# Kernel tuning notes

Hardware: AMD Instinct MI355X
Metric: run time of the kernel (lower is better)

## Reference

```python
import jax, jax.numpy as jnp
import numpy as np

N_NODES = 65536
N_EDGES = 1048576
BN_EPS = 1e-5


def _glorot(key, shape):
    fan_in, fan_out = shape[0], shape[1]
    lim = np.sqrt(6.0 / (fan_in + fan_out))
    return jax.random.uniform(key, shape, jnp.float32, -lim, lim)


def setup_inputs() -> dict:
    key = jax.random.key(0)
    ks = jax.random.split(key, 16)
    inp = {}
    inp['x'] = jax.random.normal(ks[0], (N_NODES, 3), jnp.float32)
    inp['edge_src'] = jax.random.randint(ks[1], (N_EDGES,), 0, N_NODES, jnp.int32)
    inp['edge_dst'] = jax.random.randint(ks[2], (N_EDGES,), 0, N_NODES, jnp.int32)
    inp['edge_val'] = jax.random.uniform(ks[3], (N_EDGES,), jnp.float32)
    inp['num_pts'] = 1024  # points per shape (equal-size split)
    # GraphConvolution params: out = adj @ (x @ W) + b
    inp['gc1_w'] = _glorot(ks[4], (3, 64));     inp['gc1_b'] = jnp.zeros((64,), jnp.float32)
    inp['gc2_w'] = _glorot(ks[5], (64, 64));    inp['gc2_b'] = jnp.zeros((64,), jnp.float32)
    inp['gc3_w'] = _glorot(ks[6], (64, 1024));  inp['gc3_b'] = jnp.zeros((1024,), jnp.float32)
    # MLP head: Linear(1024,512)+BN+ReLU, Linear(512,256)+BN+ReLU, Linear(256,40)
    inp['fc1_w'] = _glorot(ks[7], (1024, 512)); inp['fc1_b'] = jnp.zeros((512,), jnp.float32)
    inp['bn1_g'] = jnp.ones((512,), jnp.float32); inp['bn1_b'] = jnp.zeros((512,), jnp.float32)
    inp['fc2_w'] = _glorot(ks[8], (512, 256));  inp['fc2_b'] = jnp.zeros((256,), jnp.float32)
    inp['bn2_g'] = jnp.ones((256,), jnp.float32); inp['bn2_b'] = jnp.zeros((256,), jnp.float32)
    inp['fc3_w'] = _glorot(ks[9], (256, 40));   inp['fc3_b'] = jnp.zeros((40,), jnp.float32)
    return inp


def _gcn_layer(x, w, b, src, dst, val):
    # adj @ (x @ W) + b, adj given as COO edge list (dst <- src weighted by val)
    support = x @ w                                   # [N, F_out]
    msg = support[src] * val[:, None]                 # gather + scale
    agg = jax.ops.segment_sum(msg, dst, num_segments=N_NODES)
    return agg + b


def _batchnorm(x, gamma, beta):
    mean = jnp.mean(x, axis=0)
    var = jnp.mean(jnp.square(x - mean), axis=0)  # biased var (torch train mode)
    return (x - mean) * jax.lax.rsqrt(var + BN_EPS) * gamma + beta


def reference(x, edge_src, edge_dst, edge_val, num_pts,
              gc1_w, gc1_b, gc2_w, gc2_b, gc3_w, gc3_b,
              fc1_w, fc1_b, bn1_g, bn1_b, fc2_w, fc2_b, bn2_g, bn2_b, fc3_w, fc3_b):
    h = jax.nn.relu(_gcn_layer(x, gc1_w, gc1_b, edge_src, edge_dst, edge_val))
    h = jax.nn.relu(_gcn_layer(h, gc2_w, gc2_b, edge_src, edge_dst, edge_val))
    h = jax.nn.relu(_gcn_layer(h, gc3_w, gc3_b, edge_src, edge_dst, edge_val))
    # per-shape max pool: split into equal-size shapes along node dim
    n_shapes = N_NODES // num_pts
    global_feat = jnp.max(h.reshape(n_shapes, num_pts, 1024), axis=1)  # [B, 1024]
    # MLP head with train-mode BatchNorm
    z = jax.nn.relu(_batchnorm(global_feat @ fc1_w + fc1_b, bn1_g, bn1_b))
    z = jax.nn.relu(_batchnorm(z @ fc2_w + fc2_b, bn2_g, bn2_b))
    scores = z @ fc3_w + fc3_b                         # [B, 40]
    return jax.nn.log_softmax(scores, axis=-1)
```

## Files before the change

### kernel.cpp

```cpp
#include <hip/hip_runtime.h>
#include <math.h>

#define NN 65536
#define NE 1048576
#define CAP 17408
#define PCAP 24576

typedef __attribute__((ext_vector_type(8))) short short8;
typedef __attribute__((ext_vector_type(4))) float f32x4;

__device__ inline unsigned short f2bf(float f) {
  unsigned u = __float_as_uint(f);
  unsigned r = u + 0x7fff + ((u >> 16) & 1);
  return (unsigned short)(r >> 16);
}
__device__ inline float bf2f(unsigned short h) { return __uint_as_float(((unsigned)h) << 16); }

__global__ __launch_bounds__(256) void k_prep(const float* __restrict__ x, float4* __restrict__ x4,
                                              int* __restrict__ gcur, const float* __restrict__ w3,
                                              unsigned short* __restrict__ bfrag, unsigned* __restrict__ gf) {
  int bid = blockIdx.x, tid = threadIdx.x;
  if (bid < 256) {
    if (bid == 0 && tid < 64) gcur[tid] = 0;
    int n = bid * 256 + tid;
    x4[n] = make_float4(x[3 * n], x[3 * n + 1], x[3 * n + 2], 0.f);
  } else {
    int t = (bid - 256) * 256 + tid;
    if (t < 65536) gf[t] = 0u;
    int e = t & 7, g = (t >> 3) & 3, col = (t >> 5) & 1023, q = t >> 15;
    int k = (q & 1) * 32 + g * 8 + e;
    float v = w3[k * 1024 + col];
    unsigned short hv = f2bf(v);
    bfrag[t] = (q < 2) ? hv : f2bf(v - bf2f(hv));
  }
}

__global__ __launch_bounds__(256) void k_bin(const int* __restrict__ src, const int* __restrict__ dst,
                                             const float* __restrict__ val, int* __restrict__ gcur,
                                             uint2* __restrict__ ebin) {
  __shared__ int cnt[64], base[64];
  int tid = threadIdx.x;
  if (tid < 64) cnt[tid] = 0;
  __syncthreads();
  int e0 = blockIdx.x * 4096;
  const int4* src4 = (const int4*)(src + e0);
  const int4* dst4 = (const int4*)(dst + e0);
  const float4* val4 = (const float4*)(val + e0);
  int rsrc[16], rdst[16], rrank[16];
  float rval[16];
#pragma unroll
  for (int i = 0; i < 4; ++i) {
    int4 s4 = src4[i * 256 + tid];
    int4 d4 = dst4[i * 256 + tid];
    float4 v4 = val4[i * 256 + tid];
    rsrc[4 * i + 0] = s4.x; rsrc[4 * i + 1] = s4.y; rsrc[4 * i + 2] = s4.z; rsrc[4 * i + 3] = s4.w;
    rdst[4 * i + 0] = d4.x; rdst[4 * i + 1] = d4.y; rdst[4 * i + 2] = d4.z; rdst[4 * i + 3] = d4.w;
    rval[4 * i + 0] = v4.x; rval[4 * i + 1] = v4.y; rval[4 * i + 2] = v4.z; rval[4 * i + 3] = v4.w;
#pragma unroll
    for (int u = 0; u < 4; ++u) rrank[4 * i + u] = atomicAdd(&cnt[rdst[4 * i + u] >> 10], 1);
  }
  __syncthreads();
  if (tid < 64) base[tid] = atomicAdd(&gcur[tid], cnt[tid]);
  __syncthreads();
#pragma unroll
  for (int i = 0; i < 16; ++i) {
    int b = rdst[i] >> 10;
    ebin[b * CAP + base[b] + rrank[i]] =
        make_uint2((unsigned)rsrc[i] | ((unsigned)(rdst[i] & 1023) << 16), (unsigned)__float_as_int(rval[i]));
  }
}

__global__ __launch_bounds__(1024) void k_csr(const int* __restrict__ gcnt, const uint2* __restrict__ ebin,
                                              int2* __restrict__ offdeg, int2* __restrict__ pack) {
  __shared__ int lcnt[1024], lcur[1024];
  __shared__ int wsum[16], woff[16];
  int b = blockIdx.x, tid = threadIdx.x;
  int count = gcnt[b];
  int gbase = b * PCAP;
  lcnt[tid] = 0;
  __syncthreads();
  const uint2* eb = ebin + (size_t)b * CAP;
  for (int i0 = 0; i0 < count; i0 += 4096) {
    unsigned xs[4];
#pragma unroll
    for (int u = 0; u < 4; ++u) {
      int i = i0 + u * 1024 + tid;
      xs[u] = eb[min(i, count - 1)].x;
    }
#pragma unroll
    for (int u = 0; u < 4; ++u) {
      int i = i0 + u * 1024 + tid;
      if (i < count) atomicAdd(&lcnt[(xs[u] >> 16) & 1023], 1);
    }
  }
  __syncthreads();
  int deg = lcnt[tid];
  int pdeg = (deg + 7) & ~7;
  int lane = tid & 63, wid = tid >> 6;
  int v = pdeg;
#pragma unroll
  for (int d = 1; d < 64; d <<= 1) {
    int t = __shfl_up(v, d);
    if (lane >= d) v += t;
  }
  if (lane == 63) wsum[wid] = v;
  __syncthreads();
  if (tid < 16) {
    int s = wsum[tid];
    int sv = s;
#pragma unroll
    for (int d = 1; d < 16; d <<= 1) {
      int t = __shfl_up(sv, d);
      if (tid >= d) sv += t;
    }
    woff[tid] = sv - s;
  }
  __syncthreads();
  int o0 = woff[wid] + v - pdeg;
  lcur[tid] = o0;
  offdeg[b * 1024 + tid] = make_int2(gbase + o0, pdeg);
  __syncthreads();
  for (int i0 = 0; i0 < count; i0 += 4096) {
    uint2 es[4];
#pragma unroll
    for (int u = 0; u < 4; ++u) {
      int i = i0 + u * 1024 + tid;
      es[u] = eb[min(i, count - 1)];
    }
#pragma unroll
    for (int u = 0; u < 4; ++u) {
      int i = i0 + u * 1024 + tid;
      if (i < count) {
        int ld = (es[u].x >> 16) & 1023;
        int p = atomicAdd(&lcur[ld], 1);
        pack[gbase + p] = make_int2((int)((es[u].x & 0xffffu) << 7), (int)es[u].y);
      }
    }
  }
  int pend = o0 + pdeg;
  for (int p = o0 + deg; p < pend; ++p) pack[gbase + p] = make_int2(0, 0);
}

__global__ __launch_bounds__(256) void k_agg1(const int2* __restrict__ offdeg, const int2* __restrict__ pack,
                                              const float4* __restrict__ x4, const float* __restrict__ w,
                                              const float* __restrict__ b, unsigned short* __restrict__ out) {
  __shared__ float sw[256];
  __shared__ float sa[256][4];
  int tid = threadIdx.x;
  sw[tid] = (tid < 192) ? w[tid] : b[tid - 192];
  int n = blockIdx.x * 256 + tid;
  int2 od = offdeg[n];
  int i0 = od.x, pdeg = od.y;
  float a0 = 0.f, a1 = 0.f, a2 = 0.f;
  for (int bb = 0; bb < pdeg; bb += 8) {
    int4 p0 = *(const int4*)&pack[i0 + bb];
    int4 p1 = *(const int4*)&pack[i0 + bb + 2];
    int4 p2 = *(const int4*)&pack[i0 + bb + 4];
    int4 p3 = *(const int4*)&pack[i0 + bb + 6];
    int sx[8] = {p0.x, p0.z, p1.x, p1.z, p2.x, p2.z, p3.x, p3.z};
    int vv[8] = {p0.y, p0.w, p1.y, p1.w, p2.y, p2.w, p3.y, p3.w};
    float4 q[8];
#pragma unroll
    for (int u = 0; u < 8; ++u) q[u] = x4[(unsigned)sx[u] >> 7];
#pragma unroll
    for (int u = 0; u < 8; ++u) {
      float v = __int_as_float(vv[u]);
      a0 = fmaf(v, q[u].x, a0);
      a1 = fmaf(v, q[u].y, a1);
      a2 = fmaf(v, q[u].z, a2);
    }
  }
  sa[tid][0] = a0; sa[tid][1] = a1; sa[tid][2] = a2;
  __syncthreads();
  int j = tid & 63, g = tid >> 6;
  float wj0 = sw[j], wj1 = sw[64 + j], wj2 = sw[128 + j], bj = sw[192 + j];
  int nb = blockIdx.x * 256 + g * 64;
  for (int r = 0; r < 64; ++r) {
    float r0 = fmaf(sa[g * 64 + r][0], wj0, bj);
    r0 = fmaf(sa[g * 64 + r][1], wj1, r0);
    r0 = fmaf(sa[g * 64 + r][2], wj2, r0);
    out[(size_t)(nb + r) * 64 + j] = f2bf(fmaxf(r0, 0.f));
  }
}

__global__ __launch_bounds__(256) void k_agg64g2(const int2* __restrict__ offdeg, const int2* __restrict__ pack,
                                                 const unsigned short* __restrict__ h,
                                                 const float* __restrict__ w2, const float* __restrict__ b2,
                                                 unsigned short* __restrict__ out) {
  __shared__ float sw[64][64];
  __shared__ float rows[32][64];
  int tid = threadIdx.x;
  int lane = tid & 63, wv = tid >> 6;
  for (int t = tid; t < 1024; t += 256) ((float4*)sw)[t] = ((const float4*)w2)[t];
  __syncthreads();
  int o = lane >> 3, fl = lane & 7;
  int n = blockIdx.x * 32 + wv * 8 + o;
  int2 od = offdeg[n];
  int i0 = od.x, pdeg = od.y;
  const char* hb = (const char*)h;
  unsigned fo = (unsigned)(fl << 4);
  float c0 = 0.f, c1 = 0.f, c2 = 0.f, c3 = 0.f, c4 = 0.f, c5 = 0.f, c6 = 0.f, c7 = 0.f;
  for (int b = 0; b < pdeg; b += 8) {
    int4 p0 = *(const int4*)&pack[i0 + b];
    int4 p1 = *(const int4*)&pack[i0 + b + 2];
    int4 p2 = *(const int4*)&pack[i0 + b + 4];
    int4 p3 = *(const int4*)&pack[i0 + b + 6];
    int sx[8] = {p0.x, p0.z, p1.x, p1.z, p2.x, p2.z, p3.x, p3.z};
    int vv[8] = {p0.y, p0.w, p1.y, p1.w, p2.y, p2.w, p3.y, p3.w};
    uint4 hv[8];
#pragma unroll
    for (int u = 0; u < 8; ++u) hv[u] = *(const uint4*)(hb + ((unsigned)sx[u] + fo));
#pragma unroll
    for (int u = 0; u < 8; ++u) {
      float v = __int_as_float(vv[u]);
      c0 = fmaf(v, __uint_as_float(hv[u].x << 16), c0);
      c1 = fmaf(v, __uint_as_float(hv[u].x & 0xffff0000u), c1);
      c2 = fmaf(v, __uint_as_float(hv[u].y << 16), c2);
      c3 = fmaf(v, __uint_as_float(hv[u].y & 0xffff0000u), c3);
      c4 = fmaf(v, __uint_as_float(hv[u].z << 16), c4);
      c5 = fmaf(v, __uint_as_float(hv[u].z & 0xffff0000u), c5);
      c6 = fmaf(v, __uint_as_float(hv[u].w << 16), c6);
      c7 = fmaf(v, __uint_as_float(hv[u].w & 0xffff0000u), c7);
    }
  }
  ((float4*)rows[wv * 8 + o])[fl * 2 + 0] = make_float4(c0, c1, c2, c3);
  ((float4*)rows[wv * 8 + o])[fl * 2 + 1] = make_float4(c4, c5, c6, c7);
  int nA = blockIdx.x * 32 + wv * 8;
  float bb = b2[lane];
  float acc[8];
#pragma unroll
  for (int r = 0; r < 8; ++r) acc[r] = bb;
#pragma unroll
  for (int kk = 0; kk < 16; ++kk) {
    float w0 = sw[4 * kk + 0][lane], w1 = sw[4 * kk + 1][lane];
    float w2v = sw[4 * kk + 2][lane], w3v = sw[4 * kk + 3][lane];
#pragma unroll
    for (int r = 0; r < 8; ++r) {
      float4 qr = ((const float4*)rows[wv * 8 + r])[kk];
      acc[r] = fmaf(qr.x, w0, acc[r]);
      acc[r] = fmaf(qr.y, w1, acc[r]);
      acc[r] = fmaf(qr.z, w2v, acc[r]);
      acc[r] = fmaf(qr.w, w3v, acc[r]);
    }
  }
#pragma unroll
  for (int r = 0; r < 8; ++r)
    out[(size_t)(nA + r) * 64 + lane] = f2bf(fmaxf(acc[r], 0.f));
}

__global__ __launch_bounds__(256) void k_agg64_split(const int2* __restrict__ offdeg, const int2* __restrict__ pack,
                                                     const unsigned short* __restrict__ h,
                                                     unsigned short* __restrict__ hi,
                                                     unsigned short* __restrict__ lo) {
  int tid = threadIdx.x;
  int lane = tid & 63, wv = tid >> 6;
  int o = lane >> 3, fl = lane & 7;
  int n = blockIdx.x * 32 + wv * 8 + o;
  int2 od = offdeg[n];
  int i0 = od.x, pdeg = od.y;
  const char* hb = (const char*)h;
  unsigned fo = (unsigned)(fl << 4);
  float c0 = 0.f, c1 = 0.f, c2 = 0.f, c3 = 0.f, c4 = 0.f, c5 = 0.f, c6 = 0.f, c7 = 0.f;
  for (int b = 0; b < pdeg; b += 8) {
    int4 p0 = *(const int4*)&pack[i0 + b];
    int4 p1 = *(const int4*)&pack[i0 + b + 2];
    int4 p2 = *(const int4*)&pack[i0 + b + 4];
    int4 p3 = *(const int4*)&pack[i0 + b + 6];
    int sx[8] = {p0.x, p0.z, p1.x, p1.z, p2.x, p2.z, p3.x, p3.z};
    int vv[8] = {p0.y, p0.w, p1.y, p1.w, p2.y, p2.w, p3.y, p3.w};
    uint4 hv[8];
#pragma unroll
    for (int u = 0; u < 8; ++u) hv[u] = *(const uint4*)(hb + ((unsigned)sx[u] + fo));
#pragma unroll
    for (int u = 0; u < 8; ++u) {
      float v = __int_as_float(vv[u]);
      c0 = fmaf(v, __uint_as_float(hv[u].x << 16), c0);
      c1 = fmaf(v, __uint_as_float(hv[u].x & 0xffff0000u), c1);
      c2 = fmaf(v, __uint_as_float(hv[u].y << 16), c2);
      c3 = fmaf(v, __uint_as_float(hv[u].y & 0xffff0000u), c3);
      c4 = fmaf(v, __uint_as_float(hv[u].z << 16), c4);
      c5 = fmaf(v, __uint_as_float(hv[u].z & 0xffff0000u), c5);
      c6 = fmaf(v, __uint_as_float(hv[u].w << 16), c6);
      c7 = fmaf(v, __uint_as_float(hv[u].w & 0xffff0000u), c7);
    }
  }
  unsigned short h0 = f2bf(c0), h1 = f2bf(c1), h2 = f2bf(c2), h3 = f2bf(c3);
  unsigned short h4 = f2bf(c4), h5 = f2bf(c5), h6 = f2bf(c6), h7 = f2bf(c7);
  uint4 hiw = make_uint4((unsigned)h0 | ((unsigned)h1 << 16), (unsigned)h2 | ((unsigned)h3 << 16),
                         (unsigned)h4 | ((unsigned)h5 << 16), (unsigned)h6 | ((unsigned)h7 << 16));
  unsigned short l0 = f2bf(c0 - bf2f(h0)), l1 = f2bf(c1 - bf2f(h1));
  unsigned short l2 = f2bf(c2 - bf2f(h2)), l3 = f2bf(c3 - bf2f(h3));
  unsigned short l4 = f2bf(c4 - bf2f(h4)), l5 = f2bf(c5 - bf2f(h5));
  unsigned short l6 = f2bf(c6 - bf2f(h6)), l7 = f2bf(c7 - bf2f(h7));
  uint4 low = make_uint4((unsigned)l0 | ((unsigned)l1 << 16), (unsigned)l2 | ((unsigned)l3 << 16),
                         (unsigned)l4 | ((unsigned)l5 << 16), (unsigned)l6 | ((unsigned)l7 << 16));
  ((uint4*)hi)[(size_t)n * 8 + fl] = hiw;
  ((uint4*)lo)[(size_t)n * 8 + fl] = low;
}

__global__ __launch_bounds__(512) void k_gemm3max(const unsigned short* __restrict__ Ahi,
                                                  const unsigned short* __restrict__ Alo,
                                                  const unsigned short* __restrict__ Bfrag,
                                                  const float* __restrict__ b3,
                                                  unsigned* __restrict__ gf) {
  int b = blockIdx.x;
  int colhalf = b & 1, rowchunk = b >> 1;
  int shape = rowchunk >> 2;
  int tid = threadIdx.x;
  int wv = tid >> 6, l = tid & 63;
  int g = l >> 4, lr = l & 15;

  const short8* bf = (const short8*)Bfrag;
  int c0 = colhalf * 512 + wv * 64 + lr;
  short8 B0[4], B1[4], B2[4], B3[4];
#pragma unroll
  for (int ct = 0; ct < 4; ++ct) {
    int col = c0 + ct * 16;
    B0[ct] = bf[(0 * 1024 + col) * 4 + g];
    B1[ct] = bf[(1 * 1024 + col) * 4 + g];
    B2[ct] = bf[(2 * 1024 + col) * 4 + g];
    B3[ct] = bf[(3 * 1024 + col) * 4 + g];
  }

  float m[4] = {-1e30f, -1e30f, -1e30f, -1e30f};
  size_t abase = ((size_t)rowchunk * 256 + lr) * 64 + g * 8;
  for (int t = 0; t < 16; ++t) {
    size_t o = abase + (size_t)t * 16 * 64;
    short8 ah0 = *(const short8*)(Ahi + o);
    short8 ah1 = *(const short8*)(Ahi + o + 32);
    short8 al0 = *(const short8*)(Alo + o);
    short8 al1 = *(const short8*)(Alo + o + 32);
#pragma unroll
    for (int ct = 0; ct < 4; ++ct) {
      f32x4 acc = {0.f, 0.f, 0.f, 0.f};
      acc = __builtin_amdgcn_mfma_f32_16x16x32_bf16(ah0, B0[ct], acc, 0, 0, 0);
      acc = __builtin_amdgcn_mfma_f32_16x16x32_bf16(ah1, B1[ct], acc, 0, 0, 0);
      acc = __builtin_amdgcn_mfma_f32_16x16x32_bf16(ah0, B2[ct], acc, 0, 0, 0);
      acc = __builtin_amdgcn_mfma_f32_16x16x32_bf16(ah1, B3[ct], acc, 0, 0, 0);
      acc = __builtin_amdgcn_mfma_f32_16x16x32_bf16(al0, B0[ct], acc, 0, 0, 0);
      acc = __builtin_amdgcn_mfma_f32_16x16x32_bf16(al1, B1[ct], acc, 0, 0, 0);
      m[ct] = fmaxf(m[ct], fmaxf(fmaxf(acc[0], acc[1]), fmaxf(acc[2], acc[3])));
    }
  }
#pragma unroll
  for (int ct = 0; ct < 4; ++ct) {
    float mm = m[ct];
    mm = fmaxf(mm, __shfl_xor(mm, 16));
    mm = fmaxf(mm, __shfl_xor(mm, 32));
    if (g == 0) {
      int col = c0 + ct * 16;
      float v = fmaxf(mm + b3[col], 0.f);
      atomicMax(&gf[shape * 1024 + col], __float_as_uint(v));
    }
  }
}

__global__ __launch_bounds__(512) void k_fc(const float* __restrict__ in, const float* __restrict__ w,
                                            const float* __restrict__ bias, float* __restrict__ out,
                                            int K, int J) {
  __shared__ float sin_[1024];
  __shared__ float part[8][64];
  int jt = blockIdx.x, bb = blockIdx.y;
  int tid = threadIdx.x, s = tid >> 6, lane = tid & 63;
  for (int i = tid; i < K; i += 512) sin_[i] = in[bb * K + i];
  __syncthreads();
  int j = (jt << 6) + lane;
  int Ks = K >> 3;
  int k0 = s * Ks;
  float acc = 0.f;
  for (int k = 0; k < Ks; k += 16) {
    float wv[16];
#pragma unroll
    for (int u = 0; u < 16; ++u) wv[u] = w[(k0 + k + u) * J + j];
#pragma unroll
    for (int u = 0; u < 16; ++u) acc = fmaf(sin_[k0 + k + u], wv[u], acc);
  }
  part[s][lane] = acc;
  __syncthreads();
  if (tid < 64) {
    float r = bias[(jt << 6) + tid];
#pragma unroll
    for (int u = 0; u < 8; ++u) r += part[u][tid];
    out[bb * J + (jt << 6) + tid] = r;
  }
}

__global__ __launch_bounds__(256) void k_bn(const float* __restrict__ z, const float* __restrict__ g,
                                            const float* __restrict__ bt, float* __restrict__ out, int J) {
  __shared__ float tile[64][64];
  __shared__ float red[4][64];
  __shared__ float sc[64], sh[64];
  int tid = threadIdx.x, s = tid >> 6, lane = tid & 63;
  int j0 = blockIdx.x << 6;
  float psum = 0.f;
#pragma unroll
  for (int r = 0; r < 16; ++r) {
    int row = s * 16 + r;
    float v = z[row * J + j0 + lane];
    tile[row][lane] = v;
    psum += v;
  }
  red[s][lane] = psum;
  __syncthreads();
  if (tid < 64) sc[tid] = (red[0][tid] + red[1][tid] + red[2][tid] + red[3][tid]) * (1.f / 64.f);
  __syncthreads();
  float mean = sc[lane];
  float pv = 0.f;
#pragma unroll
  for (int r = 0; r < 16; ++r) {
    float d = tile[s * 16 + r][lane] - mean;
    pv = fmaf(d, d, pv);
  }
  red[s][lane] = pv;
  __syncthreads();
  if (tid < 64) {
    float var = (red[0][tid] + red[1][tid] + red[2][tid] + red[3][tid]) * (1.f / 64.f);
    float scale = g[j0 + tid] / sqrtf(var + 1e-5f);
    sh[tid] = bt[j0 + tid] - sc[tid] * scale;
    sc[tid] = scale;
  }
  __syncthreads();
  float scale = sc[lane], shift = sh[lane];
#pragma unroll
  for (int r = 0; r < 16; ++r) {
    int row = s * 16 + r;
    out[row * J + j0 + lane] = fmaxf(fmaf(tile[row][lane], scale, shift), 0.f);
  }
}

__global__ __launch_bounds__(256) void k_head2(const float* __restrict__ z2, const float* __restrict__ g,
                                               const float* __restrict__ bt, const float* __restrict__ w,
                                               const float* __restrict__ b, float* __restrict__ out) {
  __shared__ float sz[256];
  __shared__ float part[4][64];
  int bb = blockIdx.x, j = threadIdx.x;
  float s = 0.f;
#pragma unroll 8
  for (int r = 0; r < 64; ++r) s += z2[r * 256 + j];
  float mean = s * (1.f / 64.f);
  float v = 0.f;
#pragma unroll 8
  for (int r = 0; r < 64; ++r) {
    float d = z2[r * 256 + j] - mean;
    v = fmaf(d, d, v);
  }
  float scale = g[j] / sqrtf(v * (1.f / 64.f) + 1e-5f);
  float shift = bt[j] - mean * scale;
  sz[j] = fmaxf(fmaf(z2[bb * 256 + j], scale, shift), 0.f);
  __syncthreads();
  int sgrp = j >> 6, lane = j & 63;
  float acc = 0.f;
  if (lane < 40) {
#pragma unroll
    for (int k = 0; k < 64; k += 4) {
      int kk = sgrp * 64 + k;
      acc = fmaf(sz[kk + 0], w[(kk + 0) * 40 + lane], acc);
      acc = fmaf(sz[kk + 1], w[(kk + 1) * 40 + lane], acc);
      acc = fmaf(sz[kk + 2], w[(kk + 2) * 40 + lane], acc);
      acc = fmaf(sz[kk + 3], w[(kk + 3) * 40 + lane], acc);
    }
  }
  part[sgrp][lane] = acc;
  __syncthreads();
  if (j < 64) {
    float lv = (j < 40) ? part[0][j] + part[1][j] + part[2][j] + part[3][j] + b[j] : -INFINITY;
    float m = lv;
    for (int d = 32; d > 0; d >>= 1) m = fmaxf(m, __shfl_xor(m, d));
    float e = (j < 40) ? expf(lv - m) : 0.f;
    for (int d = 32; d > 0; d >>= 1) e += __shfl_xor(e, d);
    if (j < 40) out[bb * 40 + j] = lv - m - logf(e);
  }
}

extern "C" void kernel_launch(void* const* d_in, const int* in_sizes, int n_in,
                              void* d_out, int out_size, void* d_ws, size_t ws_size,
                              hipStream_t stream) {
  (void)in_sizes; (void)n_in; (void)out_size; (void)ws_size;
  const float* x    = (const float*)d_in[0];
  const int*   esrc = (const int*)d_in[1];
  const int*   edst = (const int*)d_in[2];
  const float* ev   = (const float*)d_in[3];
  const float* gc1w = (const float*)d_in[5];
  const float* gc1b = (const float*)d_in[6];
  const float* gc2w = (const float*)d_in[7];
  const float* gc2b = (const float*)d_in[8];
  const float* gc3w = (const float*)d_in[9];
  const float* gc3b = (const float*)d_in[10];
  const float* fc1w = (const float*)d_in[11];
  const float* fc1b = (const float*)d_in[12];
  const float* bn1g = (const float*)d_in[13];
  const float* bn1b = (const float*)d_in[14];
  const float* fc2w = (const float*)d_in[15];
  const float* fc2b = (const float*)d_in[16];
  const float* bn2g = (const float*)d_in[17];
  const float* bn2b = (const float*)d_in[18];
  const float* fc3w = (const float*)d_in[19];
  const float* fc3b = (const float*)d_in[20];

  char* ws = (char*)d_ws;
  size_t o = 0;
  auto alloc = [&](size_t bytes) -> void* {
    void* p = ws + o;
    o += (bytes + 255) & ~(size_t)255;
    return p;
  };
  int2*  offdeg = (int2*)alloc((size_t)NN * 8);
  int*   gcur = (int*)alloc(64 * 4);
  int2*  pack = (int2*)alloc((size_t)64 * PCAP * 8);
  float4* x4  = (float4*)alloc((size_t)NN * 16);
  float* bufA = (float*)alloc((size_t)NN * 64 * 4);
  float* bufB = (float*)alloc((size_t)NN * 64 * 4);
  uint2* ebin = (uint2*)bufA;
  unsigned short* h1_16 = (unsigned short*)bufA;
  unsigned short* h2_16 = (unsigned short*)((char*)bufA + NN * 64 * 2);
  unsigned short* Ahi = (unsigned short*)bufB;
  unsigned short* Alo = (unsigned short*)(bufB + NN * 32);
  unsigned short* Bfrag = (unsigned short*)alloc(4 * 1024 * 32 * 2);
  float* gf   = (float*)alloc(64 * 1024 * 4);
  float* z1   = (float*)alloc(64 * 512 * 4);
  float* z1n  = (float*)alloc(64 * 512 * 4);
  float* z2   = (float*)alloc(64 * 256 * 4);

  k_prep<<<768, 256, 0, stream>>>(x, x4, gcur, gc3w, Bfrag, (unsigned*)gf);

  k_bin<<<NE / 4096, 256, 0, stream>>>(esrc, edst, ev, gcur, ebin);
  k_csr<<<64, 1024, 0, stream>>>(gcur, ebin, offdeg, pack);

  k_agg1<<<NN / 256, 256, 0, stream>>>(offdeg, pack, x4, gc1w, gc1b, h1_16);

  k_agg64g2<<<NN / 32, 256, 0, stream>>>(offdeg, pack, h1_16, gc2w, gc2b, h2_16);

  k_agg64_split<<<NN / 32, 256, 0, stream>>>(offdeg, pack, h2_16, Ahi, Alo);
  k_gemm3max<<<512, 512, 0, stream>>>(Ahi, Alo, Bfrag, gc3b, (unsigned*)gf);

  k_fc<<<dim3(8, 64), 512, 0, stream>>>(gf, fc1w, fc1b, z1, 1024, 512);
  k_bn<<<8, 256, 0, stream>>>(z1, bn1g, bn1b, z1n, 512);
  k_fc<<<dim3(4, 64), 512, 0, stream>>>(z1n, fc2w, fc2b, z2, 512, 256);
  k_head2<<<64, 256, 0, stream>>>(z2, bn2g, bn2b, fc3w, fc3b, (float*)d_out);
}
```

Baseline: 159.4 us.

## Double-buffer neighbor gathers, cache edges in registers in CSR, fuse BN1 into fc2

The aggregation loops in the GCN layers now issue the next batch of eight neighbor loads before consuming the current batch, so gather latency overlaps with the FMAs. The CSR builder loads each bin's edges into registers once and reuses them for both the counting and scatter passes, instead of reading global memory twice. The first batchnorm is folded into the second fully connected kernel, which removes a launch and an intermediate buffer. In exchange, every fc2 block redundantly recomputes the BN statistics, and the extra buffers raise register pressure.

```diff
diff --git a/kernel.cpp b/kernel.cpp
--- a/kernel.cpp
+++ b/kernel.cpp
@@ -15,6 +15,60 @@
   return (unsigned short)(r >> 16);
 }
 __device__ inline float bf2f(unsigned short h) { return __uint_as_float(((unsigned)h) << 16); }
+
+struct HB {
+  float v[8];
+  uint4 h[8];
+};
+__device__ __forceinline__ void load_hb(const int2* __restrict__ pack, int off, const char* __restrict__ hb,
+                                        unsigned fo, HB& B) {
+  int4 p0 = *(const int4*)&pack[off];
+  int4 p1 = *(const int4*)&pack[off + 2];
+  int4 p2 = *(const int4*)&pack[off + 4];
+  int4 p3 = *(const int4*)&pack[off + 6];
+  int sx[8] = {p0.x, p0.z, p1.x, p1.z, p2.x, p2.z, p3.x, p3.z};
+  int vv[8] = {p0.y, p0.w, p1.y, p1.w, p2.y, p2.w, p3.y, p3.w};
+#pragma unroll
+  for (int u = 0; u < 8; ++u) {
+    B.v[u] = __int_as_float(vv[u]);
+    B.h[u] = *(const uint4*)(hb + ((unsigned)sx[u] + fo));
+  }
+}
+__device__ __forceinline__ void fma_hb(const HB& B, float* c) {
+#pragma unroll
+  for (int u = 0; u < 8; ++u) {
+    float v = B.v[u];
+    c[0] = fmaf(v, __uint_as_float(B.h[u].x << 16), c[0]);
+    c[1] = fmaf(v, __uint_as_float(B.h[u].x & 0xffff0000u), c[1]);
+    c[2] = fmaf(v, __uint_as_float(B.h[u].y << 16), c[2]);
+    c[3] = fmaf(v, __uint_as_float(B.h[u].y & 0xffff0000u), c[3]);
+    c[4] = fmaf(v, __uint_as_float(B.h[u].z << 16), c[4]);
+    c[5] = fmaf(v, __uint_as_float(B.h[u].z & 0xffff0000u), c[5]);
+    c[6] = fmaf(v, __uint_as_float(B.h[u].w << 16), c[6]);
+    c[7] = fmaf(v, __uint_as_float(B.h[u].w & 0xffff0000u), c[7]);
+  }
+}
+__device__ __forceinline__ void agg_pipe(const int2* __restrict__ pack, int i0, int pdeg,
+                                         const char* __restrict__ hb, unsigned fo, float* c) {
+  if (pdeg <= 0) return;
+  HB A, B;
+  load_hb(pack, i0, hb, fo, A);
+  int rounds = pdeg >> 3;
+  int r = 1;
+  for (; r + 1 < rounds; r += 2) {
+    load_hb(pack, i0 + (r << 3), hb, fo, B);
+    fma_hb(A, c);
+    load_hb(pack, i0 + ((r + 1) << 3), hb, fo, A);
+    fma_hb(B, c);
+  }
+  if (r < rounds) {
+    load_hb(pack, i0 + (r << 3), hb, fo, B);
+    fma_hb(A, c);
+    fma_hb(B, c);
+  } else {
+    fma_hb(A, c);
+  }
+}
 
 __global__ __launch_bounds__(256) void k_prep(const float* __restrict__ x, float4* __restrict__ x4,
                                               int* __restrict__ gcur, const float* __restrict__ w3,
@@ -80,19 +134,21 @@
   lcnt[tid] = 0;
   __syncthreads();
   const uint2* eb = ebin + (size_t)b * CAP;
-  for (int i0 = 0; i0 < count; i0 += 4096) {
-    unsigned xs[4];
+  uint2 es[5][4];
+#pragma unroll
+  for (int i0 = 0; i0 < 5; ++i0)
 #pragma unroll
     for (int u = 0; u < 4; ++u) {
-      int i = i0 + u * 1024 + tid;
-      xs[u] = eb[min(i, count - 1)].x;
-    }
+      int i = i0 * 4096 + u * 1024 + tid;
+      es[i0][u] = eb[min(i, count - 1)];
+    }
+#pragma unroll
+  for (int i0 = 0; i0 < 5; ++i0)
 #pragma unroll
     for (int u = 0; u < 4; ++u) {
-      int i = i0 + u * 1024 + tid;
-      if (i < count) atomicAdd(&lcnt[(xs[u] >> 16) & 1023], 1);
-    }
-  }
+      int i = i0 * 4096 + u * 1024 + tid;
+      if (i < count) atomicAdd(&lcnt[(es[i0][u].x >> 16) & 1023], 1);
+    }
   __syncthreads();
   int deg = lcnt[tid];
   int pdeg = (deg + 7) & ~7;
@@ -120,23 +176,17 @@
   lcur[tid] = o0;
   offdeg[b * 1024 + tid] = make_int2(gbase + o0, pdeg);
   __syncthreads();
-  for (int i0 = 0; i0 < count; i0 += 4096) {
-    uint2 es[4];
+#pragma unroll
+  for (int i0 = 0; i0 < 5; ++i0)
 #pragma unroll
     for (int u = 0; u < 4; ++u) {
-      int i = i0 + u * 1024 + tid;
-      es[u] = eb[min(i, count - 1)];
-    }
-#pragma unroll
-    for (int u = 0; u < 4; ++u) {
-      int i = i0 + u * 1024 + tid;
+      int i = i0 * 4096 + u * 1024 + tid;
       if (i < count) {
-        int ld = (es[u].x >> 16) & 1023;
+        int ld = (es[i0][u].x >> 16) & 1023;
         int p = atomicAdd(&lcur[ld], 1);
-        pack[gbase + p] = make_int2((int)((es[u].x & 0xffffu) << 7), (int)es[u].y);
+        pack[gbase + p] = make_int2((int)((es[i0][u].x & 0xffffu) << 7), (int)es[i0][u].y);
       }
     }
-  }
   int pend = o0 + pdeg;
   for (int p = o0 + deg; p < pend; ++p) pack[gbase + p] = make_int2(0, 0);
 }
@@ -152,22 +202,46 @@
   int2 od = offdeg[n];
   int i0 = od.x, pdeg = od.y;
   float a0 = 0.f, a1 = 0.f, a2 = 0.f;
-  for (int bb = 0; bb < pdeg; bb += 8) {
-    int4 p0 = *(const int4*)&pack[i0 + bb];
-    int4 p1 = *(const int4*)&pack[i0 + bb + 2];
-    int4 p2 = *(const int4*)&pack[i0 + bb + 4];
-    int4 p3 = *(const int4*)&pack[i0 + bb + 6];
+
+  struct XB { float v[8]; float4 q[8]; };
+  auto loadx = [&](int off, XB& B) {
+    int4 p0 = *(const int4*)&pack[off];
+    int4 p1 = *(const int4*)&pack[off + 2];
+    int4 p2 = *(const int4*)&pack[off + 4];
+    int4 p3 = *(const int4*)&pack[off + 6];
     int sx[8] = {p0.x, p0.z, p1.x, p1.z, p2.x, p2.z, p3.x, p3.z};
     int vv[8] = {p0.y, p0.w, p1.y, p1.w, p2.y, p2.w, p3.y, p3.w};
-    float4 q[8];
-#pragma unroll
-    for (int u = 0; u < 8; ++u) q[u] = x4[(unsigned)sx[u] >> 7];
 #pragma unroll
     for (int u = 0; u < 8; ++u) {
-      float v = __int_as_float(vv[u]);
-      a0 = fmaf(v, q[u].x, a0);
-      a1 = fmaf(v, q[u].y, a1);
-      a2 = fmaf(v, q[u].z, a2);
+      B.v[u] = __int_as_float(vv[u]);
+      B.q[u] = x4[(unsigned)sx[u] >> 7];
+    }
+  };
+  auto fmax_ = [&](const XB& B) {
+#pragma unroll
+    for (int u = 0; u < 8; ++u) {
+      a0 = fmaf(B.v[u], B.q[u].x, a0);
+      a1 = fmaf(B.v[u], B.q[u].y, a1);
+      a2 = fmaf(B.v[u], B.q[u].z, a2);
+    }
+  };
+  if (pdeg > 0) {
+    XB A, B;
+    loadx(i0, A);
+    int rounds = pdeg >> 3;
+    int r = 1;
+    for (; r + 1 < rounds; r += 2) {
+      loadx(i0 + (r << 3), B);
+      fmax_(A);
+      loadx(i0 + ((r + 1) << 3), A);
+      fmax_(B);
+    }
+    if (r < rounds) {
+      loadx(i0 + (r << 3), B);
+      fmax_(A);
+      fmax_(B);
+    } else {
+      fmax_(A);
     }
   }
   sa[tid][0] = a0; sa[tid][1] = a1; sa[tid][2] = a2;
@@ -196,35 +270,10 @@
   int o = lane >> 3, fl = lane & 7;
   int n = blockIdx.x * 32 + wv * 8 + o;
   int2 od = offdeg[n];
-  int i0 = od.x, pdeg = od.y;
-  const char* hb = (const char*)h;
-  unsigned fo = (unsigned)(fl << 4);
-  float c0 = 0.f, c1 = 0.f, c2 = 0.f, c3 = 0.f, c4 = 0.f, c5 = 0.f, c6 = 0.f, c7 = 0.f;
-  for (int b = 0; b < pdeg; b += 8) {
-    int4 p0 = *(const int4*)&pack[i0 + b];
-    int4 p1 = *(const int4*)&pack[i0 + b + 2];
-    int4 p2 = *(const int4*)&pack[i0 + b + 4];
-    int4 p3 = *(const int4*)&pack[i0 + b + 6];
-    int sx[8] = {p0.x, p0.z, p1.x, p1.z, p2.x, p2.z, p3.x, p3.z};
-    int vv[8] = {p0.y, p0.w, p1.y, p1.w, p2.y, p2.w, p3.y, p3.w};
-    uint4 hv[8];
-#pragma unroll
-    for (int u = 0; u < 8; ++u) hv[u] = *(const uint4*)(hb + ((unsigned)sx[u] + fo));
-#pragma unroll
-    for (int u = 0; u < 8; ++u) {
-      float v = __int_as_float(vv[u]);
-      c0 = fmaf(v, __uint_as_float(hv[u].x << 16), c0);
-      c1 = fmaf(v, __uint_as_float(hv[u].x & 0xffff0000u), c1);
-      c2 = fmaf(v, __uint_as_float(hv[u].y << 16), c2);
-      c3 = fmaf(v, __uint_as_float(hv[u].y & 0xffff0000u), c3);
-      c4 = fmaf(v, __uint_as_float(hv[u].z << 16), c4);
-      c5 = fmaf(v, __uint_as_float(hv[u].z & 0xffff0000u), c5);
-      c6 = fmaf(v, __uint_as_float(hv[u].w << 16), c6);
-      c7 = fmaf(v, __uint_as_float(hv[u].w & 0xffff0000u), c7);
-    }
-  }
-  ((float4*)rows[wv * 8 + o])[fl * 2 + 0] = make_float4(c0, c1, c2, c3);
-  ((float4*)rows[wv * 8 + o])[fl * 2 + 1] = make_float4(c4, c5, c6, c7);
+  float c[8] = {0.f, 0.f, 0.f, 0.f, 0.f, 0.f, 0.f, 0.f};
+  agg_pipe(pack, od.x, od.y, (const char*)h, (unsigned)(fl << 4), c);
+  ((float4*)rows[wv * 8 + o])[fl * 2 + 0] = make_float4(c[0], c[1], c[2], c[3]);
+  ((float4*)rows[wv * 8 + o])[fl * 2 + 1] = make_float4(c[4], c[5], c[6], c[7]);
   int nA = blockIdx.x * 32 + wv * 8;
   float bb = b2[lane];
   float acc[8];
@@ -257,41 +306,16 @@
   int o = lane >> 3, fl = lane & 7;
   int n = blockIdx.x * 32 + wv * 8 + o;
   int2 od = offdeg[n];
-  int i0 = od.x, pdeg = od.y;
-  const char* hb = (const char*)h;
-  unsigned fo = (unsigned)(fl << 4);
-  float c0 = 0.f, c1 = 0.f, c2 = 0.f, c3 = 0.f, c4 = 0.f, c5 = 0.f, c6 = 0.f, c7 = 0.f;
-  for (int b = 0; b < pdeg; b += 8) {
-    int4 p0 = *(const int4*)&pack[i0 + b];
-    int4 p1 = *(const int4*)&pack[i0 + b + 2];
-    int4 p2 = *(const int4*)&pack[i0 + b + 4];
-    int4 p3 = *(const int4*)&pack[i0 + b + 6];
-    int sx[8] = {p0.x, p0.z, p1.x, p1.z, p2.x, p2.z, p3.x, p3.z};
-    int vv[8] = {p0.y, p0.w, p1.y, p1.w, p2.y, p2.w, p3.y, p3.w};
-    uint4 hv[8];
-#pragma unroll
-    for (int u = 0; u < 8; ++u) hv[u] = *(const uint4*)(hb + ((unsigned)sx[u] + fo));
-#pragma unroll
-    for (int u = 0; u < 8; ++u) {
-      float v = __int_as_float(vv[u]);
-      c0 = fmaf(v, __uint_as_float(hv[u].x << 16), c0);
-      c1 = fmaf(v, __uint_as_float(hv[u].x & 0xffff0000u), c1);
-      c2 = fmaf(v, __uint_as_float(hv[u].y << 16), c2);
-      c3 = fmaf(v, __uint_as_float(hv[u].y & 0xffff0000u), c3);
-      c4 = fmaf(v, __uint_as_float(hv[u].z << 16), c4);
-      c5 = fmaf(v, __uint_as_float(hv[u].z & 0xffff0000u), c5);
-      c6 = fmaf(v, __uint_as_float(hv[u].w << 16), c6);
-      c7 = fmaf(v, __uint_as_float(hv[u].w & 0xffff0000u), c7);
-    }
-  }
-  unsigned short h0 = f2bf(c0), h1 = f2bf(c1), h2 = f2bf(c2), h3 = f2bf(c3);
-  unsigned short h4 = f2bf(c4), h5 = f2bf(c5), h6 = f2bf(c6), h7 = f2bf(c7);
+  float c[8] = {0.f, 0.f, 0.f, 0.f, 0.f, 0.f, 0.f, 0.f};
+  agg_pipe(pack, od.x, od.y, (const char*)h, (unsigned)(fl << 4), c);
+  unsigned short h0 = f2bf(c[0]), h1 = f2bf(c[1]), h2 = f2bf(c[2]), h3 = f2bf(c[3]);
+  unsigned short h4 = f2bf(c[4]), h5 = f2bf(c[5]), h6 = f2bf(c[6]), h7 = f2bf(c[7]);
   uint4 hiw = make_uint4((unsigned)h0 | ((unsigned)h1 << 16), (unsigned)h2 | ((unsigned)h3 << 16),
                          (unsigned)h4 | ((unsigned)h5 << 16), (unsigned)h6 | ((unsigned)h7 << 16));
-  unsigned short l0 = f2bf(c0 - bf2f(h0)), l1 = f2bf(c1 - bf2f(h1));
-  unsigned short l2 = f2bf(c2 - bf2f(h2)), l3 = f2bf(c3 - bf2f(h3));
-  unsigned short l4 = f2bf(c4 - bf2f(h4)), l5 = f2bf(c5 - bf2f(h5));
-  unsigned short l6 = f2bf(c6 - bf2f(h6)), l7 = f2bf(c7 - bf2f(h7));
+  unsigned short l0 = f2bf(c[0] - bf2f(h0)), l1 = f2bf(c[1] - bf2f(h1));
+  unsigned short l2 = f2bf(c[2] - bf2f(h2)), l3 = f2bf(c[3] - bf2f(h3));
+  unsigned short l4 = f2bf(c[4] - bf2f(h4)), l5 = f2bf(c[5] - bf2f(h5));
+  unsigned short l6 = f2bf(c[6] - bf2f(h6)), l7 = f2bf(c[7] - bf2f(h7));
   uint4 low = make_uint4((unsigned)l0 | ((unsigned)l1 << 16), (unsigned)l2 | ((unsigned)l3 << 16),
                          (unsigned)l4 | ((unsigned)l5 << 16), (unsigned)l6 | ((unsigned)l7 << 16));
   ((uint4*)hi)[(size_t)n * 8 + fl] = hiw;
@@ -385,46 +409,47 @@
   }
 }
 
-__global__ __launch_bounds__(256) void k_bn(const float* __restrict__ z, const float* __restrict__ g,
-                                            const float* __restrict__ bt, float* __restrict__ out, int J) {
-  __shared__ float tile[64][64];
-  __shared__ float red[4][64];
-  __shared__ float sc[64], sh[64];
-  int tid = threadIdx.x, s = tid >> 6, lane = tid & 63;
-  int j0 = blockIdx.x << 6;
-  float psum = 0.f;
-#pragma unroll
-  for (int r = 0; r < 16; ++r) {
-    int row = s * 16 + r;
-    float v = z[row * J + j0 + lane];
-    tile[row][lane] = v;
-    psum += v;
-  }
-  red[s][lane] = psum;
-  __syncthreads();
-  if (tid < 64) sc[tid] = (red[0][tid] + red[1][tid] + red[2][tid] + red[3][tid]) * (1.f / 64.f);
-  __syncthreads();
-  float mean = sc[lane];
-  float pv = 0.f;
-#pragma unroll
-  for (int r = 0; r < 16; ++r) {
-    float d = tile[s * 16 + r][lane] - mean;
-    pv = fmaf(d, d, pv);
-  }
-  red[s][lane] = pv;
+__global__ __launch_bounds__(512) void k_fc2n(const float* __restrict__ z1, const float* __restrict__ g1,
+                                              const float* __restrict__ be1, const float* __restrict__ w,
+                                              const float* __restrict__ bias, float* __restrict__ out) {
+  __shared__ float szn[512];
+  __shared__ float part[8][64];
+  int jt = blockIdx.x, row = blockIdx.y;
+  int tid = threadIdx.x;
+  {
+    float s = 0.f;
+#pragma unroll 8
+    for (int r = 0; r < 64; ++r) s += z1[r * 512 + tid];
+    float mean = s * (1.f / 64.f);
+    float v = 0.f;
+#pragma unroll 8
+    for (int r = 0; r < 64; ++r) {
+      float d = z1[r * 512 + tid] - mean;
+      v = fmaf(d, d, v);
+    }
+    float scale = g1[tid] / sqrtf(v * (1.f / 64.f) + 1e-5f);
+    float shift = be1[tid] - mean * scale;
+    szn[tid] = fmaxf(fmaf(z1[row * 512 + tid], scale, shift), 0.f);
+  }
+  __syncthreads();
+  int s8 = tid >> 6, lane = tid & 63;
+  int j = (jt << 6) + lane;
+  int k0 = s8 * 64;
+  float acc = 0.f;
+  for (int k = 0; k < 64; k += 16) {
+    float wv[16];
+#pragma unroll
+    for (int u = 0; u < 16; ++u) wv[u] = w[(k0 + k + u) * 256 + j];
+#pragma unroll
+    for (int u = 0; u < 16; ++u) acc = fmaf(szn[k0 + k + u], wv[u], acc);
+  }
+  part[s8][lane] = acc;
   __syncthreads();
   if (tid < 64) {
-    float var = (red[0][tid] + red[1][tid] + red[2][tid] + red[3][tid]) * (1.f / 64.f);
-    float scale = g[j0 + tid] / sqrtf(var + 1e-5f);
-    sh[tid] = bt[j0 + tid] - sc[tid] * scale;
-    sc[tid] = scale;
-  }
-  __syncthreads();
-  float scale = sc[lane], shift = sh[lane];
-#pragma unroll
-  for (int r = 0; r < 16; ++r) {
-    int row = s * 16 + r;
-    out[row * J + j0 + lane] = fmaxf(fmaf(tile[row][lane], scale, shift), 0.f);
+    float r = bias[(jt << 6) + tid];
+#pragma unroll
+    for (int u = 0; u < 8; ++u) r += part[u][tid];
+    out[row * 256 + (jt << 6) + tid] = r;
   }
 }
 
@@ -518,7 +543,6 @@
   unsigned short* Bfrag = (unsigned short*)alloc(4 * 1024 * 32 * 2);
   float* gf   = (float*)alloc(64 * 1024 * 4);
   float* z1   = (float*)alloc(64 * 512 * 4);
-  float* z1n  = (float*)alloc(64 * 512 * 4);
   float* z2   = (float*)alloc(64 * 256 * 4);
 
   k_prep<<<768, 256, 0, stream>>>(x, x4, gcur, gc3w, Bfrag, (unsigned*)gf);
@@ -534,7 +558,6 @@
   k_gemm3max<<<512, 512, 0, stream>>>(Ahi, Alo, Bfrag, gc3b, (unsigned*)gf);
 
   k_fc<<<dim3(8, 64), 512, 0, stream>>>(gf, fc1w, fc1b, z1, 1024, 512);
-  k_bn<<<8, 256, 0, stream>>>(z1, bn1g, bn1b, z1n, 512);
-  k_fc<<<dim3(4, 64), 512, 0, stream>>>(z1n, fc2w, fc2b, z2, 512, 256);
+  k_fc2n<<<dim3(4, 64), 512, 0, stream>>>(z1, bn1g, bn1b, fc2w, fc2b, z2);
   k_head2<<<64, 256, 0, stream>>>(z2, bn2g, bn2b, fc3w, fc3b, (float*)d_out);
 }
```

After: 161.1 us, median of 5. About the same (+1.1%).
